# Kernel tuning notes

Measured on AMD Instinct MI355X. Metric: run time of the kernel, lower is better.

Reference implementation:

```python
import jax, jax.numpy as jnp
import numpy as np

N, E, IN_DIM, H, D = 50000, 800000, 64, 8, 8
HD = H * D
CLAMP = 5.0


def setup_inputs() -> dict:
    key = jax.random.key(0)
    ks = jax.random.split(key, 13)
    s_in = 1.0 / np.sqrt(IN_DIM)
    s_hd = 1.0 / np.sqrt(HD)
    return {
        "x": jax.random.normal(ks[0], (N, IN_DIM), jnp.float32),
        "edge_attr": jax.random.normal(ks[1], (E, IN_DIM), jnp.float32),
        "edge_index": jax.random.randint(ks[2], (2, E), 0, N, jnp.int32),
        # torch nn.Linear weights are [out_features, in_features]
        "WQ": jax.random.normal(ks[3], (HD, IN_DIM), jnp.float32) * s_in,
        "WK": jax.random.normal(ks[4], (HD, IN_DIM), jnp.float32) * s_in,
        "WV": jax.random.normal(ks[5], (HD, IN_DIM), jnp.float32) * s_in,
        "WEw": jax.random.normal(ks[6], (HD, IN_DIM), jnp.float32) * s_in,
        "WEb": jax.random.normal(ks[7], (HD, IN_DIM), jnp.float32) * s_in,
        "bEb": jax.random.normal(ks[8], (HD,), jnp.float32) * 0.02,
        "WEo": jax.random.normal(ks[9], (HD, HD), jnp.float32) * s_hd,
        "bEo": jax.random.normal(ks[10], (HD,), jnp.float32) * 0.02,
        "Aw": jax.random.normal(ks[11], (D, H, 1), jnp.float32) * s_hd,
        "BW": jax.random.normal(ks[12], (D, H, D), jnp.float32) * s_hd,
    }


def _scatter_softmax(score, dst, num_nodes):
    # score: [E, H, 1]; softmax over edges grouped by dst node
    mx = jax.ops.segment_max(score, dst, num_segments=num_nodes)  # [N,H,1]
    ex = jnp.exp(score - mx[dst])
    den = jax.ops.segment_sum(ex, dst, num_segments=num_nodes)    # [N,H,1]
    return ex / (den[dst] + 1e-16)


def reference(x, edge_attr, edge_index, WQ, WK, WV, WEw, WEb, bEb, WEo, bEo, Aw, BW):
    n = x.shape[0]
    e = edge_attr.shape[0]
    Qh = (x @ WQ.T).reshape(n, H, D)
    Kh = (x @ WK.T).reshape(n, H, D)
    Vh = (x @ WV.T).reshape(n, H, D)
    Ew = (edge_attr @ WEw.T).reshape(e, H, D)
    Eb = (edge_attr @ WEb.T + bEb).reshape(e, H, D)

    dst, src = edge_index[0], edge_index[1]
    conn1 = (Qh[dst] + Kh[src]) * Ew                       # [E,H,D]
    # sqrt(relu(x)) - sqrt(relu(-x)) == sign(x)*sqrt(|x|)
    conn2 = jnp.sign(conn1) * jnp.sqrt(jnp.abs(conn1))
    conn = conn2 + Eb                                      # act = Identity

    Eo_flat = conn.reshape(e, HD) @ WEo.T + bEo            # Oe output [E, H*D]
    Eo = Eo_flat.reshape(e, H, D)

    score = jnp.einsum('ehd,dhc->ehc', conn, Aw)           # [E,H,1]
    score = jnp.clip(score, -CLAMP, CLAMP)
    score = _scatter_softmax(score, dst, n)

    agg = jax.ops.segment_sum(Vh[src] * score, dst, num_segments=n)   # [N,H,D]
    rowV = jax.ops.segment_sum(Eo * score, dst, num_segments=n)       # [N,H,D]
    rowV = jnp.einsum('nhd,dhc->nhc', rowV, BW)
    h_out = agg + rowV                                     # [N,H,D]
    return (h_out, Eo_flat)
```

## Files before the change

kernel.cpp:

```cpp
#include <hip/hip_runtime.h>

#define NN 50000
#define EE 800000
#define EPT 256
#define NT8 (EE / EPT)
#define NB ((NN + 1023) / 1024)

typedef __attribute__((ext_vector_type(8))) short short8;
typedef __attribute__((ext_vector_type(16))) float f32x16;

static __device__ __forceinline__ unsigned short f2bf(float f) {
    unsigned u = __float_as_uint(f);
    u += 0x7fffu + ((u >> 16) & 1u);
    return (unsigned short)(u >> 16);
}
static __device__ __forceinline__ unsigned pack2(float a, float b) {
    return (unsigned)f2bf(a) | ((unsigned)f2bf(b) << 16);
}
static __device__ __forceinline__ float bf2f(unsigned short s) {
    return __uint_as_float((unsigned)s << 16);
}
static __device__ __forceinline__ f32x16 splat16(float v) {
    f32x16 r;
    #pragma unroll
    for (int i = 0; i < 16; ++i) r[i] = v;
    return r;
}

union U8 { short8 v; uint2 u[2]; };

static __device__ __forceinline__ short8 ldsfrag(const unsigned short* rowbase, int k0) {
    U8 t;
    t.u[0] = *(const uint2*)(rowbase + k0);
    t.u[1] = *(const uint2*)(rowbase + k0 + 8);
    return t.v;
}

__global__ __launch_bounds__(256) void qkv_mfma_kernel(
    const float* __restrict__ x,
    const float* __restrict__ WQ, const float* __restrict__ WK, const float* __restrict__ WV,
    float* __restrict__ Qh, float* __restrict__ Kh, float* __restrict__ Vh)
{
    __shared__ unsigned short s_wq[64][66];
    __shared__ unsigned short s_wk[64][66];
    __shared__ unsigned short s_wv[64][66];

    int tid = threadIdx.x;
    #pragma unroll
    for (int t = 0; t < 16; ++t) {
        int idx = t * 256 + tid;
        int r = idx >> 6, c = idx & 63;
        s_wq[r][c] = f2bf(WQ[idx]);
        s_wk[r][c] = f2bf(WK[idx]);
        s_wv[r][c] = f2bf(WV[idx]);
    }
    __syncthreads();

    int wid = tid >> 6, lane = tid & 63;
    int m0 = blockIdx.x * 128 + wid * 32;
    int lo5 = lane & 31, hi = lane >> 5;

    int rowi = m0 + lo5;
    const float* arow = x + (size_t)(rowi < NN ? rowi : NN - 1) * 64;
    short8 af[4];
    #pragma unroll
    for (int ks = 0; ks < 4; ++ks) {
        int k0 = ks * 16 + hi * 4;
        float4 a0 = *(const float4*)(arow + k0);
        float4 a1 = *(const float4*)(arow + k0 + 8);
        U8 t;
        t.u[0] = make_uint2(pack2(a0.x, a0.y), pack2(a0.z, a0.w));
        t.u[1] = make_uint2(pack2(a1.x, a1.y), pack2(a1.z, a1.w));
        af[ks] = t.v;
    }

    #pragma unroll
    for (int nt = 0; nt < 2; ++nt) {
        int n = nt * 32 + lo5;
        f32x16 cQ = splat16(0.f), cK = splat16(0.f), cV = splat16(0.f);
        #pragma unroll
        for (int ks = 0; ks < 4; ++ks) {
            int k0 = ks * 16 + hi * 4;
            cQ = __builtin_amdgcn_mfma_f32_32x32x16_bf16(af[ks], ldsfrag(s_wq[n], k0), cQ, 0, 0, 0);
            cK = __builtin_amdgcn_mfma_f32_32x32x16_bf16(af[ks], ldsfrag(s_wk[n], k0), cK, 0, 0, 0);
            cV = __builtin_amdgcn_mfma_f32_32x32x16_bf16(af[ks], ldsfrag(s_wv[n], k0), cV, 0, 0, 0);
        }
        #pragma unroll
        for (int r = 0; r < 16; ++r) {
            int m = (r & 3) + 8 * (r >> 2) + 4 * hi;
            int gm = m0 + m;
            if (gm < NN) {
                Qh[(size_t)gm * 64 + n] = cQ[r];
                Kh[(size_t)gm * 64 + n] = cK[r];
                Vh[(size_t)gm * 64 + n] = cV[r];
            }
        }
    }
}

__global__ __launch_bounds__(256) void hist_kernel(const int* __restrict__ eidx,
                                                   int* __restrict__ cnt)
{
    int e = blockIdx.x * blockDim.x + threadIdx.x;
    atomicAdd(&cnt[eidx[e]], 1);
}

__global__ __launch_bounds__(1024) void scan1_kernel(const int* __restrict__ cnt,
                                                     int* __restrict__ rowstart,
                                                     int* __restrict__ bsum)
{
    __shared__ int buf[1024];
    int tid = threadIdx.x;
    int i = blockIdx.x * 1024 + tid;
    int v = (i < NN) ? cnt[i] : 0;
    buf[tid] = v;
    __syncthreads();
    for (int off = 1; off < 1024; off <<= 1) {
        int t = (tid >= off) ? buf[tid - off] : 0;
        __syncthreads();
        buf[tid] += t;
        __syncthreads();
    }
    if (i < NN) rowstart[i] = buf[tid] - v;
    if (tid == 1023) bsum[blockIdx.x] = buf[1023];
}

__global__ __launch_bounds__(64) void scan2_kernel(const int* __restrict__ bsum,
                                                   int* __restrict__ boff,
                                                   int* __restrict__ rowstart)
{
    int lane = threadIdx.x;
    int v = (lane < NB) ? bsum[lane] : 0;
    int s = v;
    #pragma unroll
    for (int off = 1; off < 64; off <<= 1) {
        int t = __shfl_up(s, off, 64);
        if (lane >= off) s += t;
    }
    if (lane < NB) boff[lane] = s - v;
    if (lane == 63) rowstart[NN] = s;
}

__global__ __launch_bounds__(1024) void scan3_kernel(int* __restrict__ rowstart,
                                                     const int* __restrict__ boff,
                                                     int* __restrict__ cursor)
{
    int i = blockIdx.x * 1024 + threadIdx.x;
    if (i < NN) {
        int r = rowstart[i] + boff[blockIdx.x];
        rowstart[i] = r;
        cursor[i] = r;
    }
}

__global__ __launch_bounds__(256) void scatter_kernel(const int* __restrict__ eidx,
                                                      int* __restrict__ cursor,
                                                      int2* __restrict__ edges_csr,
                                                      int* __restrict__ inv)
{
    int e = blockIdx.x * blockDim.x + threadIdx.x;
    int dst = eidx[e];
    int pos = atomicAdd(&cursor[dst], 1);
    edges_csr[pos] = make_int2(e, eidx[EE + e]);
    inv[e] = pos;
}

__global__ __launch_bounds__(512) void edge_mfma_kernel(
    const float* __restrict__ eattr, const int* __restrict__ eidx,
    const int* __restrict__ inv,
    const float* __restrict__ WEw, const float* __restrict__ WEb, const float* __restrict__ bEb,
    const float* __restrict__ WEo, const float* __restrict__ bEo, const float* __restrict__ Aw,
    const float* __restrict__ Qh, const float* __restrict__ Kh,
    float* __restrict__ Eo_out, float* __restrict__ exbuf)
{
    __shared__ unsigned short s_wew[64][66];
    __shared__ unsigned short s_web[64][66];
    __shared__ unsigned short s_weo[64][66];
    __shared__ unsigned short s_conn[8][32][66];

    int tid = threadIdx.x;
    #pragma unroll
    for (int t = 0; t < 8; ++t) {
        int idx = t * 512 + tid;
        int r = idx >> 6, c = idx & 63;
        s_wew[r][c] = f2bf(WEw[idx]);
        s_web[r][c] = f2bf(WEb[idx]);
        s_weo[r][c] = f2bf(WEo[idx]);
    }
    __syncthreads();

    int wid = tid >> 6, lane = tid & 63;
    int lo5 = lane & 31, hi = lane >> 5;

    float awv[32];
    #pragma unroll
    for (int ks = 0; ks < 4; ++ks)
        #pragma unroll
        for (int i = 0; i < 8; ++i) {
            int k = ks * 16 + hi * 4 + (i & 3) + ((i >> 2) << 3);
            awv[ks * 8 + i] = Aw[(k & 7) * 8 + (k >> 3)];
        }
    float bEbn0 = bEb[lo5], bEbn1 = bEb[32 + lo5];
    float bEon0 = bEo[lo5], bEon1 = bEo[32 + lo5];

    for (int tile = blockIdx.x; tile < NT8; tile += gridDim.x) {
        int e0 = tile * EPT + wid * 32;
        int pos = inv[e0 + lo5];

        short8 af[4];
        {
            const float* arow = eattr + (size_t)(e0 + lo5) * 64;
            #pragma unroll
            for (int ks = 0; ks < 4; ++ks) {
                int k0 = ks * 16 + hi * 4;
                float4 a0 = *(const float4*)(arow + k0);
                float4 a1 = *(const float4*)(arow + k0 + 8);
                U8 t;
                t.u[0] = make_uint2(pack2(a0.x, a0.y), pack2(a0.z, a0.w));
                t.u[1] = make_uint2(pack2(a1.x, a1.y), pack2(a1.z, a1.w));
                af[ks] = t.v;
            }
        }

        #pragma unroll
        for (int nt = 0; nt < 2; ++nt) {
            int n = nt * 32 + lo5;

            float qk[16];
            #pragma unroll
            for (int rr = 0; rr < 4; ++rr) {
                int4 d4 = *(const int4*)(eidx + e0 + rr * 8 + hi * 4);
                int4 s4 = *(const int4*)(eidx + EE + e0 + rr * 8 + hi * 4);
                qk[rr * 4 + 0] = Qh[(size_t)d4.x * 64 + n] + Kh[(size_t)s4.x * 64 + n];
                qk[rr * 4 + 1] = Qh[(size_t)d4.y * 64 + n] + Kh[(size_t)s4.y * 64 + n];
                qk[rr * 4 + 2] = Qh[(size_t)d4.z * 64 + n] + Kh[(size_t)s4.z * 64 + n];
                qk[rr * 4 + 3] = Qh[(size_t)d4.w * 64 + n] + Kh[(size_t)s4.w * 64 + n];
            }

            f32x16 cEw = splat16(0.f), cEb = splat16(0.f);
            #pragma unroll
            for (int ks = 0; ks < 4; ++ks) {
                int k0 = ks * 16 + hi * 4;
                cEw = __builtin_amdgcn_mfma_f32_32x32x16_bf16(af[ks], ldsfrag(s_wew[n], k0), cEw, 0, 0, 0);
                cEb = __builtin_amdgcn_mfma_f32_32x32x16_bf16(af[ks], ldsfrag(s_web[n], k0), cEb, 0, 0, 0);
            }
            float bEbn = nt ? bEbn1 : bEbn0;
            #pragma unroll
            for (int r = 0; r < 16; ++r) {
                int m = (r & 3) + 8 * (r >> 2) + 4 * hi;
                float c1 = qk[r] * cEw[r];
                float c2 = copysignf(sqrtf(fabsf(c1)), c1);
                s_conn[wid][m][n] = f2bf(c2 + cEb[r] + bEbn);
            }
        }

        short8 ca[4];
        #pragma unroll
        for (int ks = 0; ks < 4; ++ks) {
            int k0 = ks * 16 + hi * 4;
            ca[ks] = ldsfrag(s_conn[wid][lo5], k0);
        }

        {
            float sc[8];
            #pragma unroll
            for (int h2 = 0; h2 < 8; ++h2) sc[h2] = 0.f;
            #pragma unroll
            for (int ks = 0; ks < 4; ++ks)
                #pragma unroll
                for (int i = 0; i < 8; ++i) {
                    float cv = bf2f((unsigned short)ca[ks][i]);
                    sc[2 * ks + (i >> 2)] = fmaf(cv, awv[ks * 8 + i], sc[2 * ks + (i >> 2)]);
                }
            #pragma unroll
            for (int h2 = 0; h2 < 8; ++h2) {
                sc[h2] += __shfl_xor(sc[h2], 32, 64);
                sc[h2] = fminf(fmaxf(sc[h2], -5.0f), 5.0f);
                sc[h2] = __expf(sc[h2]);
            }
            if (hi == 0) {
                *(float4*)(exbuf + (size_t)pos * 8 + 0) = make_float4(sc[0], sc[1], sc[2], sc[3]);
                *(float4*)(exbuf + (size_t)pos * 8 + 4) = make_float4(sc[4], sc[5], sc[6], sc[7]);
            }
        }

        #pragma unroll
        for (int nt = 0; nt < 2; ++nt) {
            int n = nt * 32 + lo5;
            f32x16 cO = splat16(nt ? bEon1 : bEon0);
            #pragma unroll
            for (int ks = 0; ks < 4; ++ks) {
                int k0 = ks * 16 + hi * 4;
                cO = __builtin_amdgcn_mfma_f32_32x32x16_bf16(ca[ks], ldsfrag(s_weo[n], k0), cO, 0, 0, 0);
            }
            #pragma unroll
            for (int r = 0; r < 16; ++r) {
                int m = (r & 3) + 8 * (r >> 2) + 4 * hi;
                Eo_out[(size_t)(e0 + m) * 64 + n] = cO[r];
            }
        }
    }
}

__global__ __launch_bounds__(256) void node_kernel(
    const int* __restrict__ rowstart, const int2* __restrict__ edges_csr,
    const float* __restrict__ exbuf, const float* __restrict__ Eo,
    const float* __restrict__ Vh, const float* __restrict__ BW,
    float* __restrict__ hout)
{
    int n = (blockIdx.x * blockDim.x + threadIdx.x) >> 6;
    int lane = threadIdx.x & 63;
    int h = lane >> 3, d = lane & 7;

    int beg = rowstart[n], end = rowstart[n + 1];
    float agg0 = 0.f, rv0 = 0.f, den0 = 0.f;
    float agg1 = 0.f, rv1 = 0.f, den1 = 0.f;
    int j = beg;
    for (; j + 1 < end; j += 2) {
        int2 ea = edges_csr[j];
        int2 eb = edges_csr[j + 1];
        float xa = exbuf[(size_t)j * 8 + h];
        float xb = exbuf[(size_t)(j + 1) * 8 + h];
        agg0 = fmaf(xa, Vh[(size_t)ea.y * 64 + lane], agg0);
        rv0  = fmaf(xa, Eo[(size_t)ea.x * 64 + lane], rv0);
        den0 += xa;
        agg1 = fmaf(xb, Vh[(size_t)eb.y * 64 + lane], agg1);
        rv1  = fmaf(xb, Eo[(size_t)eb.x * 64 + lane], rv1);
        den1 += xb;
    }
    if (j < end) {
        int2 ea = edges_csr[j];
        float xa = exbuf[(size_t)j * 8 + h];
        agg0 = fmaf(xa, Vh[(size_t)ea.y * 64 + lane], agg0);
        rv0  = fmaf(xa, Eo[(size_t)ea.x * 64 + lane], rv0);
        den0 += xa;
    }
    float agg = agg0 + agg1, rv = rv0 + rv1, den = den0 + den1;
    float inv = (den > 0.f) ? (1.0f / den) : 0.f;

    float acc = agg;
    #pragma unroll
    for (int dd = 0; dd < 8; ++dd) {
        float rvd = __shfl(rv, (h << 3) + dd, 64);
        acc = fmaf(rvd, BW[dd * 64 + (h << 3) + d], acc);
    }
    hout[(size_t)n * 64 + lane] = acc * inv;
}

extern "C" void kernel_launch(void* const* d_in, const int* in_sizes, int n_in,
                              void* d_out, int out_size, void* d_ws, size_t ws_size,
                              hipStream_t stream)
{
    const float* x    = (const float*)d_in[0];
    const float* ea   = (const float*)d_in[1];
    const int*   eidx = (const int*)  d_in[2];
    const float* WQ   = (const float*)d_in[3];
    const float* WK   = (const float*)d_in[4];
    const float* WV   = (const float*)d_in[5];
    const float* WEw  = (const float*)d_in[6];
    const float* WEb  = (const float*)d_in[7];
    const float* bEb  = (const float*)d_in[8];
    const float* WEo  = (const float*)d_in[9];
    const float* bEo  = (const float*)d_in[10];
    const float* Aw   = (const float*)d_in[11];
    const float* BW   = (const float*)d_in[12];

    float* hout   = (float*)d_out;
    float* Eo_out = hout + (size_t)NN * 64;

    float* Qh    = (float*)d_ws;
    float* Kh    = Qh + (size_t)NN * 64;
    float* Vh    = Kh + (size_t)NN * 64;
    float* exbuf = Vh + (size_t)NN * 64;
    int* cnt      = (int*)(exbuf + (size_t)EE * 8);
    int* rowstart = cnt + NN;
    int2* edges_csr = (int2*)(rowstart + NN + 2);
    int* invp     = (int*)(edges_csr + EE);
    int* bsum     = invp + EE;
    int* boff     = bsum + 64;

    hipMemsetAsync(cnt, 0, (size_t)NN * sizeof(int), stream);

    hist_kernel<<<EE / 256, 256, 0, stream>>>(eidx, cnt);
    scan1_kernel<<<NB, 1024, 0, stream>>>(cnt, rowstart, bsum);
    scan2_kernel<<<1, 64, 0, stream>>>(bsum, boff, rowstart);
    scan3_kernel<<<NB, 1024, 0, stream>>>(rowstart, boff, cnt);
    scatter_kernel<<<EE / 256, 256, 0, stream>>>(eidx, cnt, edges_csr, invp);

    qkv_mfma_kernel<<<(NN + 127) / 128, 256, 0, stream>>>(x, WQ, WK, WV, Qh, Kh, Vh);

    edge_mfma_kernel<<<512, 512, 0, stream>>>(ea, eidx, invp, WEw, WEb, bEb, WEo, bEo, Aw,
                                              Qh, Kh, Eo_out, exbuf);

    node_kernel<<<(NN * 64) / 256, 256, 0, stream>>>(rowstart, edges_csr,
                                                     exbuf, Eo_out, Vh, BW, hout);
}
```

Measured before the change: 386.2 us.

## Transpose edge MFMA layout to keep conn in registers and vectorize gathers

Swaps the MFMA operand order so each lane owns one edge's output features. This lets conn be packed into bf16 A-fragments directly in registers, which removes the shared-memory round trip through s_conn. The Q/K gathers and Eo stores become float4 row accesses instead of scalar strided ones. The per-head score reduction now runs as an extra MFMA against a block-diagonal Aw matrix held in LDS. The persistent grid-stride loop is replaced by one 256-edge tile per block, and the launch grid grows to match. Trade-offs are more block launches, repeated per-block weight staging into LDS, and one extra MFMA chain per tile.

```diff
diff --git a/kernel.cpp b/kernel.cpp
--- a/kernel.cpp
+++ b/kernel.cpp
@@ -2,8 +2,6 @@
 
 #define NN 50000
 #define EE 800000
-#define EPT 256
-#define NT8 (EE / EPT)
 #define NB ((NN + 1023) / 1024)
 
 typedef __attribute__((ext_vector_type(8))) short short8;
@@ -16,9 +14,6 @@
 }
 static __device__ __forceinline__ unsigned pack2(float a, float b) {
     return (unsigned)f2bf(a) | ((unsigned)f2bf(b) << 16);
-}
-static __device__ __forceinline__ float bf2f(unsigned short s) {
-    return __uint_as_float((unsigned)s << 16);
 }
 static __device__ __forceinline__ f32x16 splat16(float v) {
     f32x16 r;
@@ -176,7 +171,9 @@
     __shared__ unsigned short s_wew[64][66];
     __shared__ unsigned short s_web[64][66];
     __shared__ unsigned short s_weo[64][66];
-    __shared__ unsigned short s_conn[8][32][66];
+    __shared__ unsigned short s_baw[32][66];
+    __shared__ float s_bEb[64];
+    __shared__ float s_bEo[64];
 
     int tid = threadIdx.x;
     #pragma unroll
@@ -187,117 +184,114 @@
         s_web[r][c] = f2bf(WEb[idx]);
         s_weo[r][c] = f2bf(WEo[idx]);
     }
+    #pragma unroll
+    for (int t = 0; t < 4; ++t) {
+        int idx = t * 512 + tid;
+        int n = idx >> 6, k = idx & 63;
+        s_baw[n][k] = (n == (k >> 3)) ? f2bf(Aw[(k & 7) * 8 + n]) : (unsigned short)0;
+    }
+    if (tid < 64) { s_bEb[tid] = bEb[tid]; s_bEo[tid] = bEo[tid]; }
     __syncthreads();
 
     int wid = tid >> 6, lane = tid & 63;
     int lo5 = lane & 31, hi = lane >> 5;
 
-    float awv[32];
-    #pragma unroll
-    for (int ks = 0; ks < 4; ++ks)
-        #pragma unroll
-        for (int i = 0; i < 8; ++i) {
-            int k = ks * 16 + hi * 4 + (i & 3) + ((i >> 2) << 3);
-            awv[ks * 8 + i] = Aw[(k & 7) * 8 + (k >> 3)];
-        }
-    float bEbn0 = bEb[lo5], bEbn1 = bEb[32 + lo5];
-    float bEon0 = bEo[lo5], bEon1 = bEo[32 + lo5];
-
-    for (int tile = blockIdx.x; tile < NT8; tile += gridDim.x) {
-        int e0 = tile * EPT + wid * 32;
-        int pos = inv[e0 + lo5];
-
-        short8 af[4];
-        {
-            const float* arow = eattr + (size_t)(e0 + lo5) * 64;
+    int e = blockIdx.x * 256 + wid * 32 + lo5;
+    int dst = eidx[e], src = eidx[EE + e], pos = inv[e];
+
+    short8 af[4];
+    {
+        const float* arow = eattr + (size_t)e * 64;
+        #pragma unroll
+        for (int ks = 0; ks < 4; ++ks) {
+            int k0 = ks * 16 + hi * 4;
+            float4 a0 = *(const float4*)(arow + k0);
+            float4 a1 = *(const float4*)(arow + k0 + 8);
+            U8 t;
+            t.u[0] = make_uint2(pack2(a0.x, a0.y), pack2(a0.z, a0.w));
+            t.u[1] = make_uint2(pack2(a1.x, a1.y), pack2(a1.z, a1.w));
+            af[ks] = t.v;
+        }
+    }
+
+    short8 ca[4];
+    #pragma unroll
+    for (int nt = 0; nt < 2; ++nt) {
+        float qk[16];
+        #pragma unroll
+        for (int r4 = 0; r4 < 4; ++r4) {
+            int off = nt * 32 + r4 * 8 + hi * 4;
+            float4 qv = *(const float4*)(Qh + (size_t)dst * 64 + off);
+            float4 kv = *(const float4*)(Kh + (size_t)src * 64 + off);
+            qk[r4 * 4 + 0] = qv.x + kv.x;
+            qk[r4 * 4 + 1] = qv.y + kv.y;
+            qk[r4 * 4 + 2] = qv.z + kv.z;
+            qk[r4 * 4 + 3] = qv.w + kv.w;
+        }
+
+        f32x16 cEw = splat16(0.f), cEb = splat16(0.f);
+        #pragma unroll
+        for (int ks = 0; ks < 4; ++ks) {
+            int k0 = ks * 16 + hi * 4;
+            short8 wf = ldsfrag(s_wew[nt * 32 + lo5], k0);
+            short8 bf = ldsfrag(s_web[nt * 32 + lo5], k0);
+            cEw = __builtin_amdgcn_mfma_f32_32x32x16_bf16(wf, af[ks], cEw, 0, 0, 0);
+            cEb = __builtin_amdgcn_mfma_f32_32x32x16_bf16(bf, af[ks], cEb, 0, 0, 0);
+        }
+
+        float conn[16];
+        #pragma unroll
+        for (int r4 = 0; r4 < 4; ++r4) {
+            float4 bb = *(const float4*)&s_bEb[nt * 32 + r4 * 8 + hi * 4];
+            float bbv[4] = {bb.x, bb.y, bb.z, bb.w};
             #pragma unroll
-            for (int ks = 0; ks < 4; ++ks) {
-                int k0 = ks * 16 + hi * 4;
-                float4 a0 = *(const float4*)(arow + k0);
-                float4 a1 = *(const float4*)(arow + k0 + 8);
-                U8 t;
-                t.u[0] = make_uint2(pack2(a0.x, a0.y), pack2(a0.z, a0.w));
-                t.u[1] = make_uint2(pack2(a1.x, a1.y), pack2(a1.z, a1.w));
-                af[ks] = t.v;
-            }
-        }
-
-        #pragma unroll
-        for (int nt = 0; nt < 2; ++nt) {
-            int n = nt * 32 + lo5;
-
-            float qk[16];
-            #pragma unroll
-            for (int rr = 0; rr < 4; ++rr) {
-                int4 d4 = *(const int4*)(eidx + e0 + rr * 8 + hi * 4);
-                int4 s4 = *(const int4*)(eidx + EE + e0 + rr * 8 + hi * 4);
-                qk[rr * 4 + 0] = Qh[(size_t)d4.x * 64 + n] + Kh[(size_t)s4.x * 64 + n];
-                qk[rr * 4 + 1] = Qh[(size_t)d4.y * 64 + n] + Kh[(size_t)s4.y * 64 + n];
-                qk[rr * 4 + 2] = Qh[(size_t)d4.z * 64 + n] + Kh[(size_t)s4.z * 64 + n];
-                qk[rr * 4 + 3] = Qh[(size_t)d4.w * 64 + n] + Kh[(size_t)s4.w * 64 + n];
-            }
-
-            f32x16 cEw = splat16(0.f), cEb = splat16(0.f);
-            #pragma unroll
-            for (int ks = 0; ks < 4; ++ks) {
-                int k0 = ks * 16 + hi * 4;
-                cEw = __builtin_amdgcn_mfma_f32_32x32x16_bf16(af[ks], ldsfrag(s_wew[n], k0), cEw, 0, 0, 0);
-                cEb = __builtin_amdgcn_mfma_f32_32x32x16_bf16(af[ks], ldsfrag(s_web[n], k0), cEb, 0, 0, 0);
-            }
-            float bEbn = nt ? bEbn1 : bEbn0;
-            #pragma unroll
-            for (int r = 0; r < 16; ++r) {
-                int m = (r & 3) + 8 * (r >> 2) + 4 * hi;
+            for (int c = 0; c < 4; ++c) {
+                int r = r4 * 4 + c;
                 float c1 = qk[r] * cEw[r];
                 float c2 = copysignf(sqrtf(fabsf(c1)), c1);
-                s_conn[wid][m][n] = f2bf(c2 + cEb[r] + bEbn);
+                conn[r] = c2 + cEb[r] + bbv[c];
             }
         }
 
-        short8 ca[4];
-        #pragma unroll
-        for (int ks = 0; ks < 4; ++ks) {
-            int k0 = ks * 16 + hi * 4;
-            ca[ks] = ldsfrag(s_conn[wid][lo5], k0);
-        }
-
-        {
-            float sc[8];
-            #pragma unroll
-            for (int h2 = 0; h2 < 8; ++h2) sc[h2] = 0.f;
-            #pragma unroll
-            for (int ks = 0; ks < 4; ++ks)
-                #pragma unroll
-                for (int i = 0; i < 8; ++i) {
-                    float cv = bf2f((unsigned short)ca[ks][i]);
-                    sc[2 * ks + (i >> 2)] = fmaf(cv, awv[ks * 8 + i], sc[2 * ks + (i >> 2)]);
-                }
-            #pragma unroll
-            for (int h2 = 0; h2 < 8; ++h2) {
-                sc[h2] += __shfl_xor(sc[h2], 32, 64);
-                sc[h2] = fminf(fmaxf(sc[h2], -5.0f), 5.0f);
-                sc[h2] = __expf(sc[h2]);
-            }
-            if (hi == 0) {
-                *(float4*)(exbuf + (size_t)pos * 8 + 0) = make_float4(sc[0], sc[1], sc[2], sc[3]);
-                *(float4*)(exbuf + (size_t)pos * 8 + 4) = make_float4(sc[4], sc[5], sc[6], sc[7]);
-            }
-        }
-
-        #pragma unroll
-        for (int nt = 0; nt < 2; ++nt) {
-            int n = nt * 32 + lo5;
-            f32x16 cO = splat16(nt ? bEon1 : bEon0);
-            #pragma unroll
-            for (int ks = 0; ks < 4; ++ks) {
-                int k0 = ks * 16 + hi * 4;
-                cO = __builtin_amdgcn_mfma_f32_32x32x16_bf16(ca[ks], ldsfrag(s_weo[n], k0), cO, 0, 0, 0);
-            }
-            #pragma unroll
-            for (int r = 0; r < 16; ++r) {
-                int m = (r & 3) + 8 * (r >> 2) + 4 * hi;
-                Eo_out[(size_t)(e0 + m) * 64 + n] = cO[r];
-            }
+        U8 t0, t1;
+        t0.u[0] = make_uint2(pack2(conn[0], conn[1]), pack2(conn[2], conn[3]));
+        t0.u[1] = make_uint2(pack2(conn[4], conn[5]), pack2(conn[6], conn[7]));
+        t1.u[0] = make_uint2(pack2(conn[8], conn[9]), pack2(conn[10], conn[11]));
+        t1.u[1] = make_uint2(pack2(conn[12], conn[13]), pack2(conn[14], conn[15]));
+        ca[2 * nt + 0] = t0.v;
+        ca[2 * nt + 1] = t1.v;
+    }
+
+    {
+        f32x16 cS = splat16(0.f);
+        #pragma unroll
+        for (int ks = 0; ks < 4; ++ks) {
+            int k0 = ks * 16 + hi * 4;
+            cS = __builtin_amdgcn_mfma_f32_32x32x16_bf16(ldsfrag(s_baw[lo5], k0), ca[ks], cS, 0, 0, 0);
+        }
+        float4 exv;
+        exv.x = __expf(fminf(fmaxf(cS[0], -5.0f), 5.0f));
+        exv.y = __expf(fminf(fmaxf(cS[1], -5.0f), 5.0f));
+        exv.z = __expf(fminf(fmaxf(cS[2], -5.0f), 5.0f));
+        exv.w = __expf(fminf(fmaxf(cS[3], -5.0f), 5.0f));
+        *(float4*)(exbuf + (size_t)pos * 8 + hi * 4) = exv;
+    }
+
+    #pragma unroll
+    for (int nt = 0; nt < 2; ++nt) {
+        f32x16 cO = splat16(0.f);
+        #pragma unroll
+        for (int ks = 0; ks < 4; ++ks) {
+            int k0 = ks * 16 + hi * 4;
+            cO = __builtin_amdgcn_mfma_f32_32x32x16_bf16(ldsfrag(s_weo[nt * 32 + lo5], k0), ca[ks], cO, 0, 0, 0);
+        }
+        #pragma unroll
+        for (int r4 = 0; r4 < 4; ++r4) {
+            int off = nt * 32 + r4 * 8 + hi * 4;
+            float4 bo = *(const float4*)&s_bEo[off];
+            float4 o = make_float4(cO[r4 * 4 + 0] + bo.x, cO[r4 * 4 + 1] + bo.y,
+                                   cO[r4 * 4 + 2] + bo.z, cO[r4 * 4 + 3] + bo.w);
+            *(float4*)(Eo_out + (size_t)e * 64 + off) = o;
         }
     }
 }
@@ -389,8 +383,8 @@
 
     qkv_mfma_kernel<<<(NN + 127) / 128, 256, 0, stream>>>(x, WQ, WK, WV, Qh, Kh, Vh);
 
-    edge_mfma_kernel<<<512, 512, 0, stream>>>(ea, eidx, invp, WEw, WEb, bEb, WEo, bEo, Aw,
-                                              Qh, Kh, Eo_out, exbuf);
+    edge_mfma_kernel<<<EE / 256, 512, 0, stream>>>(ea, eidx, invp, WEw, WEb, bEb,
+                                                   WEo, bEo, Aw, Qh, Kh, Eo_out, exbuf);
 
     node_kernel<<<(NN * 64) / 256, 256, 0, stream>>>(rowstart, edges_csr,
                                                      exbuf, Eo_out, Vh, BW, hout);
```

Result: slower. 422.4 us (+9.4%).
